# Performance work log

Hardware: AMD Instinct MI355X
Metric: run time of the kernel (lower is better)

## Reference

```python
import jax, jax.numpy as jnp
import numpy as np

B, S, H, NH, L, MLP_MULT = 4, 1024, 1024, 16, 2, 4
DK = H // NH
EPS = 1e-5


def setup_inputs() -> dict:
    key = jax.random.key(0)
    ks = jax.random.split(key, 8)
    p = lambda k, shape: jax.random.normal(k, shape, dtype=jnp.float32) * 0.02
    return {
        'hidden_states': jax.random.normal(ks[0], (B, S, H), dtype=jnp.float32),
        'attn_w': p(ks[1], (L, H, 3 * H)),
        'attn_b': jnp.zeros((L, 3 * H), jnp.float32),
        'proj_w': p(ks[2], (L, H, H)),
        'proj_b': jnp.zeros((L, H), jnp.float32),
        'fc_w': p(ks[3], (L, H, MLP_MULT * H)),
        'fc_b': jnp.zeros((L, MLP_MULT * H), jnp.float32),
        'fc2_w': p(ks[4], (L, MLP_MULT * H, H)),
        'fc2_b': jnp.zeros((L, H), jnp.float32),
        'ln1_g': jnp.ones((L, H), jnp.float32),
        'ln1_b': jnp.zeros((L, H), jnp.float32),
        'ln2_g': jnp.ones((L, H), jnp.float32),
        'ln2_b': jnp.zeros((L, H), jnp.float32),
        'position_ids': jnp.arange(S, dtype=jnp.int32),
    }


def _ln(x, g, b):
    m = jnp.mean(x, axis=-1, keepdims=True)
    v = jnp.var(x, axis=-1, keepdims=True)
    return (x - m) * jax.lax.rsqrt(v + EPS) * g + b


def _rotate_half(x):
    x1, x2 = jnp.split(x, 2, axis=-1)
    return jnp.concatenate((-x2, x1), axis=-1)


def _forward(hidden_states, attn_w, attn_b, proj_w, proj_b, fc_w, fc_b,
             fc2_w, fc2_b, ln1_g, ln1_b, ln2_g, ln2_b, position_ids):
    # rotary tables (fp32 math, as in RotaryEmbedding.forward)
    inv_freq = 1.0 / (10000.0 ** (jnp.arange(0, DK, 2, dtype=jnp.float32) / DK))
    freqs = position_ids.astype(jnp.float32)[:, None] * inv_freq[None, :]  # [S, DK/2]
    emb = jnp.concatenate((freqs, freqs), axis=-1)                          # [S, DK]
    cos = jnp.cos(emb)[None, None]  # [1,1,S,DK]
    sin = jnp.sin(emb)[None, None]
    causal = jnp.tril(jnp.ones((S, S), dtype=bool))
    neg = jnp.finfo(jnp.float32).min
    scale = 1.0 / np.sqrt(DK).astype(np.float32)

    h = hidden_states
    for i in range(L):
        # attention block
        x = _ln(h, ln1_g[i], ln1_b[i])
        qkv = x @ attn_w[i] + attn_b[i]                  # Conv1D c_attn
        q, k, v = jnp.split(qkv, 3, axis=-1)
        heads = lambda t: t.reshape(B, S, NH, DK).transpose(0, 2, 1, 3)
        q, k, v = heads(q), heads(k), heads(v)           # [B,NH,S,DK]
        q = q * cos + _rotate_half(q) * sin
        k = k * cos + _rotate_half(k) * sin
        # fp32 QK^T (baddbmm with alpha=scale, beta=0)
        w = jnp.einsum('bhqd,bhkd->bhqk', q.astype(jnp.float32),
                       k.astype(jnp.float32)) * scale    # [B,NH,S,S]
        w = jnp.where(causal, w, neg)
        w = jax.nn.softmax(w, axis=-1).astype(v.dtype)   # attn dropout is identity (eval)
        a = jnp.einsum('bhqk,bhkd->bhqd', w, v)
        a = a.transpose(0, 2, 1, 3).reshape(B, S, H)     # merge_heads
        h = h + (a @ proj_w[i] + proj_b[i])              # c_proj + residual
        # MLP block (gelu_new == tanh-approx gelu)
        x = _ln(h, ln2_g[i], ln2_b[i])
        mid = jax.nn.gelu(x @ fc_w[i] + fc_b[i], approximate=True)
        h = h + (mid @ fc2_w[i] + fc2_b[i])
    return h


def reference(hidden_states, attn_w, attn_b, proj_w, proj_b, fc_w, fc_b,
              fc2_w, fc2_b, ln1_g, ln1_b, ln2_g, ln2_b, position_ids):
    return _forward(hidden_states, attn_w, attn_b, proj_w, proj_b, fc_w, fc_b,
                    fc2_w, fc2_b, ln1_g, ln1_b, ln2_g, ln2_b, position_ids)
```

## Files before the change

### kernel.cpp

```cpp
#include <hip/hip_runtime.h>

#define B_ 4
#define S_ 1024
#define H_ 1024
#define NH_ 16
#define DK_ 64
#define MLPH_ 4096
#define EPS_ 1e-5f

typedef __attribute__((ext_vector_type(8))) short short8_t;
typedef __attribute__((ext_vector_type(8))) unsigned short ushort8_t;
typedef __attribute__((ext_vector_type(4))) float f32x4;

__device__ __forceinline__ unsigned short f2bf(float f) {
  unsigned int u = __float_as_uint(f);
  u = u + 0x7fffu + ((u >> 16) & 1u);
  return (unsigned short)(u >> 16);
}
__device__ __forceinline__ float bf2f(unsigned short b) {
  return __uint_as_float(((unsigned int)b) << 16);
}

__device__ __forceinline__ void gload16(const void* g, void* l) {
  typedef const __attribute__((address_space(1))) unsigned int GU;
  typedef __attribute__((address_space(3))) unsigned int LU;
  __builtin_amdgcn_global_load_lds((GU*)(size_t)g, (LU*)(unsigned int)(size_t)l, 16, 0, 0);
}

__device__ __forceinline__ float gelu_tanh(float x) {
  float y = 1.5957691216057308f * (x + 0.044715f * x * x * x);
  return x / (1.0f + __expf(-y));
}

__global__ __launch_bounds__(256) void wconv(const float* __restrict__ src,
                                             unsigned short* __restrict__ dst,
                                             int K, int N) {
  __shared__ float t[32][33];
  int n0 = blockIdx.x * 32, k0 = blockIdx.y * 32;
  int tid = threadIdx.x;
  int r = tid >> 3, c = (tid & 7) * 4;
  const float* s = src + (size_t)(k0 + r) * N + n0 + c;
  float4 v = *(const float4*)s;
  t[r][c] = v.x; t[r][c + 1] = v.y; t[r][c + 2] = v.z; t[r][c + 3] = v.w;
  __syncthreads();
  ushort4 o;
  o.x = f2bf(t[c + 0][r]); o.y = f2bf(t[c + 1][r]);
  o.z = f2bf(t[c + 2][r]); o.w = f2bf(t[c + 3][r]);
  *(ushort4*)(dst + (size_t)(n0 + r) * K + k0 + c) = o;
}

__global__ __launch_bounds__(256) void ln_kernel(const float* __restrict__ x,
                                                 const float* __restrict__ g,
                                                 const float* __restrict__ b,
                                                 unsigned short* __restrict__ y) {
  int row = blockIdx.x, tid = threadIdx.x;
  const float* xp = x + (size_t)row * H_;
  float4 v = *((const float4*)xp + tid);
  float s  = v.x + v.y + v.z + v.w;
  float s2 = v.x * v.x + v.y * v.y + v.z * v.z + v.w * v.w;
  #pragma unroll
  for (int o = 1; o < 64; o <<= 1) {
    s  += __shfl_xor(s, o, 64);
    s2 += __shfl_xor(s2, o, 64);
  }
  __shared__ float r1[4], r2[4];
  if ((tid & 63) == 0) { r1[tid >> 6] = s; r2[tid >> 6] = s2; }
  __syncthreads();
  s  = r1[0] + r1[1] + r1[2] + r1[3];
  s2 = r2[0] + r2[1] + r2[2] + r2[3];
  float mean = s * (1.0f / H_);
  float var  = s2 * (1.0f / H_) - mean * mean;
  float inv  = rsqrtf(var + EPS_);
  float4 gv = *((const float4*)g + tid);
  float4 bv = *((const float4*)b + tid);
  ushort4 o;
  o.x = f2bf((v.x - mean) * inv * gv.x + bv.x);
  o.y = f2bf((v.y - mean) * inv * gv.y + bv.y);
  o.z = f2bf((v.z - mean) * inv * gv.z + bv.z);
  o.w = f2bf((v.w - mean) * inv * gv.w + bv.w);
  *(ushort4*)(y + (size_t)row * H_ + tid * 4) = o;
}

__global__ __launch_bounds__(256) void rope_bf(unsigned short* qkv, const int* __restrict__ pos) {
  int idx = blockIdx.x * 256 + threadIdx.x;
  int d = idx & 31;
  int hh = (idx >> 5) & 15;
  int s = (idx >> 9) & 1023;
  int b = idx >> 19;
  size_t base = ((size_t)(b * S_ + s)) * 3072 + hh * 64;
  float inv = __expf(-9.210340371976184f * ((float)d * 0.03125f));
  float th = (float)pos[s] * inv;
  float cs = cosf(th), sn = sinf(th);
  unsigned short* qp = qkv + base;
  unsigned short* kp = qkv + base + 1024;
  float q0 = bf2f(qp[d]), q1 = bf2f(qp[d + 32]);
  float k0 = bf2f(kp[d]), k1 = bf2f(kp[d + 32]);
  qp[d]      = f2bf(q0 * cs - q1 * sn);
  qp[d + 32] = f2bf(q1 * cs + q0 * sn);
  kp[d]      = f2bf(k0 * cs - k1 * sn);
  kp[d + 32] = f2bf(k1 * cs + k0 * sn);
}

template <int MODE, int NT>
__global__ __launch_bounds__(256) void gemm_mfma(
    const unsigned short* __restrict__ A, const unsigned short* __restrict__ Bt,
    const float* __restrict__ bias, const float* __restrict__ resid,
    void* __restrict__ outp, int M, int N, int K) {
  constexpr int BN = NT * 32;
  constexpr int CB = BN / 32;
  __shared__ __align__(16) unsigned short As[2][128 * 64];
  __shared__ __align__(16) unsigned short Bs[2][BN * 64];
  int tid = threadIdx.x;
  int w = tid >> 6, lane = tid & 63;
  int m0 = blockIdx.y * 128, n0 = blockIdx.x * BN;
  int wr = w >> 1, wc = w & 1;
  int fr = lane & 15, kg = lane >> 4;
  f32x4 acc[4][NT];
  #pragma unroll
  for (int m = 0; m < 4; m++)
    #pragma unroll
    for (int n = 0; n < NT; n++) {
      acc[m][n][0] = 0.f; acc[m][n][1] = 0.f; acc[m][n][2] = 0.f; acc[m][n][3] = 0.f;
    }
  int srow = lane >> 3;
  int scol = ((lane & 7) ^ srow) * 8;
  const unsigned short* Ap = A  + (size_t)(m0 + w * 32 + srow) * K + scol;
  const unsigned short* Bp = Bt + (size_t)(n0 + w * (8 * CB) + srow) * K + scol;
  int sx = (fr & 7);
  int nk = K >> 6;
  {
    char* AsB = (char*)As[0] + w * 4096;
    char* BsB = (char*)Bs[0] + w * CB * 1024;
    #pragma unroll
    for (int i = 0; i < 4; i++) gload16(Ap + (size_t)i * 8 * K, AsB + i * 1024);
    #pragma unroll
    for (int i = 0; i < CB; i++) gload16(Bp + (size_t)i * 8 * K, BsB + i * 1024);
  }
  __syncthreads();
  for (int t = 0; t < nk; t++) {
    int cur = t & 1;
    if (t + 1 < nk) {
      const unsigned short* Ap2 = Ap + (size_t)(t + 1) * 64;
      const unsigned short* Bp2 = Bp + (size_t)(t + 1) * 64;
      char* AsB = (char*)As[cur ^ 1] + w * 4096;
      char* BsB = (char*)Bs[cur ^ 1] + w * CB * 1024;
      #pragma unroll
      for (int i = 0; i < 4; i++) gload16(Ap2 + (size_t)i * 8 * K, AsB + i * 1024);
      #pragma unroll
      for (int i = 0; i < CB; i++) gload16(Bp2 + (size_t)i * 8 * K, BsB + i * 1024);
    }
    #pragma unroll
    for (int kk = 0; kk < 2; kk++) {
      int slot = ((kk * 4 + kg) ^ sx) << 4;
      short8_t af[4], bfr[NT];
      #pragma unroll
      for (int m = 0; m < 4; m++)
        af[m] = *(const short8_t*)((char*)As[cur] + (wr * 64 + m * 16 + fr) * 128 + slot);
      #pragma unroll
      for (int n = 0; n < NT; n++)
        bfr[n] = *(const short8_t*)((char*)Bs[cur] + (wc * (NT * 16) + n * 16 + fr) * 128 + slot);
      #pragma unroll
      for (int m = 0; m < 4; m++)
        #pragma unroll
        for (int n = 0; n < NT; n++)
          acc[m][n] = __builtin_amdgcn_mfma_f32_16x16x32_bf16(af[m], bfr[n], acc[m][n], 0, 0, 0);
    }
    __syncthreads();
  }
  #pragma unroll
  for (int n = 0; n < NT; n++) {
    int col = n0 + wc * (NT * 16) + n * 16 + fr;
    float bv = bias[col];
    #pragma unroll
    for (int m = 0; m < 4; m++) {
      int row = m0 + wr * 64 + m * 16 + kg * 4;
      #pragma unroll
      for (int r = 0; r < 4; r++) {
        float v = acc[m][n][r] + bv;
        size_t idx = (size_t)(row + r) * N + col;
        if (MODE == 2)      ((float*)outp)[idx] = resid[idx] + v;
        else if (MODE == 1) ((unsigned short*)outp)[idx] = f2bf(gelu_tanh(v));
        else                ((unsigned short*)outp)[idx] = f2bf(v);
      }
    }
  }
}

__global__ __launch_bounds__(256) void attn3(const unsigned short* __restrict__ qkv,
                                             unsigned short* __restrict__ aout) {
  __shared__ __align__(16) unsigned short Ks[2][64 * 64];
  __shared__ __align__(16) unsigned short Vt[2][64 * 64];
  __shared__ __align__(16) unsigned short Ps[4][16 * 64];
  int tid = threadIdx.x;
  int w = tid >> 6, lane = tid & 63;
  int fr = lane & 15, kg = lane >> 4;
  int qt = (int)gridDim.x - 1 - (int)blockIdx.x;
  int q0 = qt * 64;
  int head = blockIdx.y, b = blockIdx.z;
  const unsigned short* base = qkv + ((size_t)b * S_) * 3072 + head * 64;

  const unsigned short* qp = base + (size_t)(q0 + w * 16 + fr) * 3072 + kg * 8;
  short8_t qa0 = *(const short8_t*)qp;
  short8_t qa1 = *(const short8_t*)(qp + 32);

  f32x4 acc[4];
  float mrun[4], lrun[4];
  #pragma unroll
  for (int n = 0; n < 4; n++) { acc[n][0] = 0.f; acc[n][1] = 0.f; acc[n][2] = 0.f; acc[n][3] = 0.f; }
  #pragma unroll
  for (int r = 0; r < 4; r++) { mrun[r] = -3.0e38f; lrun[r] = 0.f; }

  int skv = lane;
  int sd0 = w * 16;

  const unsigned short* kp0 = base + 1024 + (size_t)skv * 3072 + sd0;
  short8_t ka = *(const short8_t*)kp0;
  short8_t kb = *(const short8_t*)(kp0 + 8);
  short8_t va = *(const short8_t*)(kp0 + 1024);
  short8_t vb = *(const short8_t*)(kp0 + 1032);

  for (int t = 0; t <= qt; t++) {
    int cur = t & 1;
    {
      unsigned kbyte = skv * 128 + sd0 * 2;
      unsigned ksw = (skv & 7) << 4;
      *(short8_t*)((char*)Ks[cur] + (kbyte ^ ksw)) = ka;
      *(short8_t*)((char*)Ks[cur] + ((kbyte + 16) ^ ksw)) = kb;
      #pragma unroll
      for (int j = 0; j < 8; j++) {
        int d0 = sd0 + j, d1 = sd0 + 8 + j;
        *(unsigned short*)((char*)Vt[cur] + ((d0 * 128 + skv * 2) ^ ((d0 & 7) << 4))) = (unsigned short)va[j];
        *(unsigned short*)((char*)Vt[cur] + ((d1 * 128 + skv * 2) ^ ((d1 & 7) << 4))) = (unsigned short)vb[j];
      }
    }
    if (t < qt) {
      const unsigned short* kp = base + 1024 + (size_t)((t + 1) * 64 + skv) * 3072 + sd0;
      ka = *(const short8_t*)kp;
      kb = *(const short8_t*)(kp + 8);
      va = *(const short8_t*)(kp + 1024);
      vb = *(const short8_t*)(kp + 1032);
    }
    __syncthreads();
    f32x4 s[4];
    #pragma unroll
    for (int n = 0; n < 4; n++) {
      int kvrow = n * 16 + fr;
      unsigned sw = (kvrow & 7) << 4;
      short8_t b0 = *(const short8_t*)((char*)Ks[cur] + ((kvrow * 128 + kg * 16) ^ sw));
      short8_t b1 = *(const short8_t*)((char*)Ks[cur] + ((kvrow * 128 + 64 + kg * 16) ^ sw));
      f32x4 z; z[0] = 0.f; z[1] = 0.f; z[2] = 0.f; z[3] = 0.f;
      z = __builtin_amdgcn_mfma_f32_16x16x32_bf16(qa0, b0, z, 0, 0, 0);
      z = __builtin_amdgcn_mfma_f32_16x16x32_bf16(qa1, b1, z, 0, 0, 0);
      s[n] = z;
    }
    bool diag = (t == qt);
    float p[4][4], pmax[4];
    #pragma unroll
    for (int r = 0; r < 4; r++) {
      int qrow = w * 16 + kg * 4 + r;
      float rm = -3.0e38f;
      #pragma unroll
      for (int n = 0; n < 4; n++) {
        float sv = s[n][r] * 0.125f;
        if (diag && (n * 16 + fr > qrow)) sv = -3.0e38f;
        s[n][r] = sv;
        rm = fmaxf(rm, sv);
      }
      pmax[r] = rm;
    }
    bool need = (pmax[0] > mrun[0] + 8.f) | (pmax[1] > mrun[1] + 8.f) |
                (pmax[2] > mrun[2] + 8.f) | (pmax[3] > mrun[3] + 8.f);
    if (__any(need)) {
      #pragma unroll
      for (int r = 0; r < 4; r++) {
        float rm = pmax[r];
        rm = fmaxf(rm, __shfl_xor(rm, 1, 64));
        rm = fmaxf(rm, __shfl_xor(rm, 2, 64));
        rm = fmaxf(rm, __shfl_xor(rm, 4, 64));
        rm = fmaxf(rm, __shfl_xor(rm, 8, 64));
        float mn = fmaxf(mrun[r], rm);
        float sc = __expf(mrun[r] - mn);
        mrun[r] = mn;
        lrun[r] *= sc;
        #pragma unroll
        for (int n = 0; n < 4; n++) acc[n][r] *= sc;
      }
    }
    #pragma unroll
    for (int r = 0; r < 4; r++) {
      float ls = 0.f;
      #pragma unroll
      for (int n = 0; n < 4; n++) {
        float e = __expf(s[n][r] - mrun[r]);
        p[n][r] = e;
        ls += e;
      }
      lrun[r] += ls;
    }
    #pragma unroll
    for (int n = 0; n < 4; n++)
      #pragma unroll
      for (int r = 0; r < 4; r++) {
        int row = kg * 4 + r, col = n * 16 + fr;
        *(unsigned short*)((char*)Ps[w] + ((row * 128 + col * 2) ^ ((row & 7) << 4))) = f2bf(p[n][r]);
      }
    asm volatile("s_waitcnt lgkmcnt(0)" ::: "memory");
    unsigned psw = (fr & 7) << 4;
    short8_t pa0 = *(const short8_t*)((char*)Ps[w] + ((fr * 128 + kg * 16) ^ psw));
    short8_t pa1 = *(const short8_t*)((char*)Ps[w] + ((fr * 128 + 64 + kg * 16) ^ psw));
    #pragma unroll
    for (int n = 0; n < 4; n++) {
      int d = n * 16 + fr;
      unsigned sw = (d & 7) << 4;
      short8_t v0 = *(const short8_t*)((char*)Vt[cur] + ((d * 128 + kg * 16) ^ sw));
      short8_t v1 = *(const short8_t*)((char*)Vt[cur] + ((d * 128 + 64 + kg * 16) ^ sw));
      acc[n] = __builtin_amdgcn_mfma_f32_16x16x32_bf16(pa0, v0, acc[n], 0, 0, 0);
      acc[n] = __builtin_amdgcn_mfma_f32_16x16x32_bf16(pa1, v1, acc[n], 0, 0, 0);
    }
  }
  #pragma unroll
  for (int r = 0; r < 4; r++) {
    float ls = lrun[r];
    ls += __shfl_xor(ls, 1, 64);
    ls += __shfl_xor(ls, 2, 64);
    ls += __shfl_xor(ls, 4, 64);
    ls += __shfl_xor(ls, 8, 64);
    float inv = 1.0f / ls;
    size_t row = (size_t)b * S_ + q0 + w * 16 + kg * 4 + r;
    unsigned short* op = aout + row * H_ + head * 64 + fr;
    #pragma unroll
    for (int n = 0; n < 4; n++) op[n * 16] = f2bf(acc[n][r] * inv);
  }
}

extern "C" void kernel_launch(void* const* d_in, const int* in_sizes, int n_in,
                              void* d_out, int out_size, void* d_ws, size_t ws_size,
                              hipStream_t stream) {
  const float* hs     = (const float*)d_in[0];
  const float* attn_w = (const float*)d_in[1];
  const float* attn_b = (const float*)d_in[2];
  const float* proj_w = (const float*)d_in[3];
  const float* proj_b = (const float*)d_in[4];
  const float* fc_w   = (const float*)d_in[5];
  const float* fc_b   = (const float*)d_in[6];
  const float* fc2_w  = (const float*)d_in[7];
  const float* fc2_b  = (const float*)d_in[8];
  const float* ln1_g  = (const float*)d_in[9];
  const float* ln1_b  = (const float*)d_in[10];
  const float* ln2_g  = (const float*)d_in[11];
  const float* ln2_b  = (const float*)d_in[12];
  const int*   pos    = (const int*)d_in[13];

  float* hres = (float*)d_out;
  const size_t rows = (size_t)B_ * S_;

  unsigned short* wQ    = (unsigned short*)d_ws;
  unsigned short* wP    = wQ  + (size_t)2 * 3072 * 1024;
  unsigned short* wF1   = wP  + (size_t)2 * 1024 * 1024;
  unsigned short* wF2   = wF1 + (size_t)2 * 4096 * 1024;
  unsigned short* xbf   = wF2 + (size_t)2 * 1024 * 4096;
  unsigned short* qkvbf = xbf + rows * H_;
  unsigned short* midbf = qkvbf + rows * 3 * H_;
  unsigned short* aoutbf= midbf + rows * MLPH_;

  hipMemcpyAsync(hres, hs, rows * H_ * sizeof(float), hipMemcpyDeviceToDevice, stream);

  for (int l = 0; l < 2; l++) {
    wconv<<<dim3(96, 32), 256, 0, stream>>>(attn_w + (size_t)l * 1024 * 3072,
                                            wQ + (size_t)l * 3072 * 1024, 1024, 3072);
    wconv<<<dim3(32, 32), 256, 0, stream>>>(proj_w + (size_t)l * 1024 * 1024,
                                            wP + (size_t)l * 1024 * 1024, 1024, 1024);
    wconv<<<dim3(128, 32), 256, 0, stream>>>(fc_w + (size_t)l * 1024 * 4096,
                                             wF1 + (size_t)l * 4096 * 1024, 1024, 4096);
    wconv<<<dim3(32, 128), 256, 0, stream>>>(fc2_w + (size_t)l * 4096 * 1024,
                                             wF2 + (size_t)l * 1024 * 4096, 4096, 1024);
  }

  for (int l = 0; l < 2; l++) {
    ln_kernel<<<rows, 256, 0, stream>>>(hres, ln1_g + l * H_, ln1_b + l * H_, xbf);
    gemm_mfma<0, 4><<<dim3(24, 32), 256, 0, stream>>>(
        xbf, wQ + (size_t)l * 3072 * 1024, attn_b + (size_t)l * 3072, nullptr,
        qkvbf, 4096, 3072, 1024);
    rope_bf<<<8192, 256, 0, stream>>>(qkvbf, pos);
    attn3<<<dim3(16, 16, 4), 256, 0, stream>>>(qkvbf, aoutbf);
    gemm_mfma<2, 2><<<dim3(16, 32), 256, 0, stream>>>(
        aoutbf, wP + (size_t)l * 1024 * 1024, proj_b + (size_t)l * 1024, hres,
        hres, 4096, 1024, 1024);
    ln_kernel<<<rows, 256, 0, stream>>>(hres, ln2_g + l * H_, ln2_b + l * H_, xbf);
    gemm_mfma<1, 4><<<dim3(32, 32), 256, 0, stream>>>(
        xbf, wF1 + (size_t)l * 4096 * 1024, fc_b + (size_t)l * 4096, nullptr,
        midbf, 4096, 4096, 1024);
    gemm_mfma<2, 2><<<dim3(16, 32), 256, 0, stream>>>(
        midbf, wF2 + (size_t)l * 1024 * 4096, fc2_b + (size_t)l * 1024, hres,
        hres, 4096, 1024, 4096);
  }
}
```

Before: 478.7 us.

## Load K fragments directly to registers in attention, add XCD tile swizzle and setprio

The attention kernel drops the K shared-memory tile. Each wave now loads its own K MFMA fragments straight from global memory into registers and prefetches the next tile after the QK MFMAs, which removes LDS writes and reads for K. It also wraps the MFMA sections in s_setprio to favour the matrix work. Separately, the GEMM remaps block IDs with an 8-way XCD-aware swizzle to improve L2 locality of tiles across chiplets, at the cost of redundant K global loads across the four waves.

```diff
diff --git a/kernel.cpp b/kernel.cpp
--- a/kernel.cpp
+++ b/kernel.cpp
@@ -112,7 +112,12 @@
   __shared__ __align__(16) unsigned short Bs[2][BN * 64];
   int tid = threadIdx.x;
   int w = tid >> 6, lane = tid & 63;
-  int m0 = blockIdx.y * 128, n0 = blockIdx.x * BN;
+  int gx = gridDim.x;
+  int nwg = gx * gridDim.y;
+  int bid = blockIdx.y * gx + blockIdx.x;
+  int cpx = nwg >> 3;
+  int swz = (bid & 7) * cpx + (bid >> 3);
+  int m0 = (swz / gx) * 128, n0 = (swz % gx) * BN;
   int wr = w >> 1, wc = w & 1;
   int fr = lane & 15, kg = lane >> 4;
   f32x4 acc[4][NT];
@@ -186,9 +191,8 @@
   }
 }
 
-__global__ __launch_bounds__(256) void attn3(const unsigned short* __restrict__ qkv,
+__global__ __launch_bounds__(256) void attn4(const unsigned short* __restrict__ qkv,
                                              unsigned short* __restrict__ aout) {
-  __shared__ __align__(16) unsigned short Ks[2][64 * 64];
   __shared__ __align__(16) unsigned short Vt[2][64 * 64];
   __shared__ __align__(16) unsigned short Ps[4][16 * 64];
   int tid = threadIdx.x;
@@ -212,46 +216,53 @@
 
   int skv = lane;
   int sd0 = w * 16;
-
-  const unsigned short* kp0 = base + 1024 + (size_t)skv * 3072 + sd0;
-  short8_t ka = *(const short8_t*)kp0;
-  short8_t kb = *(const short8_t*)(kp0 + 8);
-  short8_t va = *(const short8_t*)(kp0 + 1024);
-  short8_t vb = *(const short8_t*)(kp0 + 1032);
+  const unsigned short* vbase = base + 2048;
+  const size_t KSTRIDE = (size_t)64 * 3072;
+
+  const unsigned short* kfp0 = base + 1024 + (size_t)(0 * 16 + fr) * 3072 + kg * 8;
+  const unsigned short* kfp1 = base + 1024 + (size_t)(1 * 16 + fr) * 3072 + kg * 8;
+  const unsigned short* kfp2 = base + 1024 + (size_t)(2 * 16 + fr) * 3072 + kg * 8;
+  const unsigned short* kfp3 = base + 1024 + (size_t)(3 * 16 + fr) * 3072 + kg * 8;
+
+  short8_t kf0[4], kf1[4];
+  kf0[0] = *(const short8_t*)kfp0;  kf1[0] = *(const short8_t*)(kfp0 + 32);
+  kf0[1] = *(const short8_t*)kfp1;  kf1[1] = *(const short8_t*)(kfp1 + 32);
+  kf0[2] = *(const short8_t*)kfp2;  kf1[2] = *(const short8_t*)(kfp2 + 32);
+  kf0[3] = *(const short8_t*)kfp3;  kf1[3] = *(const short8_t*)(kfp3 + 32);
+  const unsigned short* vp0 = vbase + (size_t)skv * 3072 + sd0;
+  short8_t va = *(const short8_t*)vp0;
+  short8_t vb = *(const short8_t*)(vp0 + 8);
 
   for (int t = 0; t <= qt; t++) {
     int cur = t & 1;
-    {
-      unsigned kbyte = skv * 128 + sd0 * 2;
-      unsigned ksw = (skv & 7) << 4;
-      *(short8_t*)((char*)Ks[cur] + (kbyte ^ ksw)) = ka;
-      *(short8_t*)((char*)Ks[cur] + ((kbyte + 16) ^ ksw)) = kb;
-      #pragma unroll
-      for (int j = 0; j < 8; j++) {
-        int d0 = sd0 + j, d1 = sd0 + 8 + j;
-        *(unsigned short*)((char*)Vt[cur] + ((d0 * 128 + skv * 2) ^ ((d0 & 7) << 4))) = (unsigned short)va[j];
-        *(unsigned short*)((char*)Vt[cur] + ((d1 * 128 + skv * 2) ^ ((d1 & 7) << 4))) = (unsigned short)vb[j];
-      }
+    #pragma unroll
+    for (int j = 0; j < 8; j++) {
+      int d0 = sd0 + j, d1 = sd0 + 8 + j;
+      *(unsigned short*)((char*)Vt[cur] + ((d0 * 128 + skv * 2) ^ ((d0 & 7) << 4))) = (unsigned short)va[j];
+      *(unsigned short*)((char*)Vt[cur] + ((d1 * 128 + skv * 2) ^ ((d1 & 7) << 4))) = (unsigned short)vb[j];
     }
     if (t < qt) {
-      const unsigned short* kp = base + 1024 + (size_t)((t + 1) * 64 + skv) * 3072 + sd0;
-      ka = *(const short8_t*)kp;
-      kb = *(const short8_t*)(kp + 8);
-      va = *(const short8_t*)(kp + 1024);
-      vb = *(const short8_t*)(kp + 1032);
+      const unsigned short* vp = vbase + (size_t)((t + 1) * 64 + skv) * 3072 + sd0;
+      va = *(const short8_t*)vp;
+      vb = *(const short8_t*)(vp + 8);
     }
     __syncthreads();
+    __builtin_amdgcn_s_setprio(1);
     f32x4 s[4];
     #pragma unroll
     for (int n = 0; n < 4; n++) {
-      int kvrow = n * 16 + fr;
-      unsigned sw = (kvrow & 7) << 4;
-      short8_t b0 = *(const short8_t*)((char*)Ks[cur] + ((kvrow * 128 + kg * 16) ^ sw));
-      short8_t b1 = *(const short8_t*)((char*)Ks[cur] + ((kvrow * 128 + 64 + kg * 16) ^ sw));
       f32x4 z; z[0] = 0.f; z[1] = 0.f; z[2] = 0.f; z[3] = 0.f;
-      z = __builtin_amdgcn_mfma_f32_16x16x32_bf16(qa0, b0, z, 0, 0, 0);
-      z = __builtin_amdgcn_mfma_f32_16x16x32_bf16(qa1, b1, z, 0, 0, 0);
+      z = __builtin_amdgcn_mfma_f32_16x16x32_bf16(qa0, kf0[n], z, 0, 0, 0);
+      z = __builtin_amdgcn_mfma_f32_16x16x32_bf16(qa1, kf1[n], z, 0, 0, 0);
       s[n] = z;
+    }
+    __builtin_amdgcn_s_setprio(0);
+    if (t < qt) {
+      size_t off = (size_t)(t + 1) * KSTRIDE;
+      kf0[0] = *(const short8_t*)(kfp0 + off);  kf1[0] = *(const short8_t*)(kfp0 + off + 32);
+      kf0[1] = *(const short8_t*)(kfp1 + off);  kf1[1] = *(const short8_t*)(kfp1 + off + 32);
+      kf0[2] = *(const short8_t*)(kfp2 + off);  kf1[2] = *(const short8_t*)(kfp2 + off + 32);
+      kf0[3] = *(const short8_t*)(kfp3 + off);  kf1[3] = *(const short8_t*)(kfp3 + off + 32);
     }
     bool diag = (t == qt);
     float p[4][4], pmax[4];
@@ -308,6 +319,7 @@
     unsigned psw = (fr & 7) << 4;
     short8_t pa0 = *(const short8_t*)((char*)Ps[w] + ((fr * 128 + kg * 16) ^ psw));
     short8_t pa1 = *(const short8_t*)((char*)Ps[w] + ((fr * 128 + 64 + kg * 16) ^ psw));
+    __builtin_amdgcn_s_setprio(1);
     #pragma unroll
     for (int n = 0; n < 4; n++) {
       int d = n * 16 + fr;
@@ -317,6 +329,7 @@
       acc[n] = __builtin_amdgcn_mfma_f32_16x16x32_bf16(pa0, v0, acc[n], 0, 0, 0);
       acc[n] = __builtin_amdgcn_mfma_f32_16x16x32_bf16(pa1, v1, acc[n], 0, 0, 0);
     }
+    __builtin_amdgcn_s_setprio(0);
   }
   #pragma unroll
   for (int r = 0; r < 4; r++) {
@@ -382,7 +395,7 @@
         xbf, wQ + (size_t)l * 3072 * 1024, attn_b + (size_t)l * 3072, nullptr,
         qkvbf, 4096, 3072, 1024);
     rope_bf<<<8192, 256, 0, stream>>>(qkvbf, pos);
-    attn3<<<dim3(16, 16, 4), 256, 0, stream>>>(qkvbf, aoutbf);
+    attn4<<<dim3(16, 16, 4), 256, 0, stream>>>(qkvbf, aoutbf);
     gemm_mfma<2, 2><<<dim3(16, 32), 256, 0, stream>>>(
         aoutbf, wP + (size_t)l * 1024 * 1024, proj_b + (size_t)l * 1024, hres,
         hres, 4096, 1024, 1024);
```

New measurement: 523.6 us. 1.09x slower.

## Enlarge attention query tile to 128 rows and swizzle GEMM workgroups across XCDs

Applied to the files above, without the earlier changes.

The attention kernel now gives each block 128 query rows, two 16-row groups per wave, so each K/V tile staged in shared memory is reused by twice as many MFMAs, and the grid is halved. MFMA sections are wrapped in s_setprio to favour matrix issue. The GEMM remaps block IDs in groups of eight so consecutive tiles land on the same XCD for better L2 locality. In exchange the attention kernel uses more registers and has fewer blocks, which can hurt occupancy and causal load balance.

```diff
diff --git a/kernel.cpp b/kernel.cpp
--- a/kernel.cpp
+++ b/kernel.cpp
@@ -112,7 +112,12 @@
   __shared__ __align__(16) unsigned short Bs[2][BN * 64];
   int tid = threadIdx.x;
   int w = tid >> 6, lane = tid & 63;
-  int m0 = blockIdx.y * 128, n0 = blockIdx.x * BN;
+  int gx = gridDim.x;
+  int nwg = gx * gridDim.y;
+  int bid = blockIdx.y * gx + blockIdx.x;
+  int cpx = nwg >> 3;
+  int swz = (bid & 7) * cpx + (bid >> 3);
+  int m0 = (swz / gx) * 128, n0 = (swz % gx) * BN;
   int wr = w >> 1, wc = w & 1;
   int fr = lane & 15, kg = lane >> 4;
   f32x4 acc[4][NT];
@@ -186,29 +191,36 @@
   }
 }
 
-__global__ __launch_bounds__(256) void attn3(const unsigned short* __restrict__ qkv,
+__global__ __launch_bounds__(256) void attn5(const unsigned short* __restrict__ qkv,
                                              unsigned short* __restrict__ aout) {
   __shared__ __align__(16) unsigned short Ks[2][64 * 64];
   __shared__ __align__(16) unsigned short Vt[2][64 * 64];
-  __shared__ __align__(16) unsigned short Ps[4][16 * 64];
+  __shared__ __align__(16) unsigned short Ps[4][2][16 * 64];
   int tid = threadIdx.x;
   int w = tid >> 6, lane = tid & 63;
   int fr = lane & 15, kg = lane >> 4;
   int qt = (int)gridDim.x - 1 - (int)blockIdx.x;
-  int q0 = qt * 64;
+  int q0 = qt * 128;
   int head = blockIdx.y, b = blockIdx.z;
   const unsigned short* base = qkv + ((size_t)b * S_) * 3072 + head * 64;
 
-  const unsigned short* qp = base + (size_t)(q0 + w * 16 + fr) * 3072 + kg * 8;
-  short8_t qa0 = *(const short8_t*)qp;
-  short8_t qa1 = *(const short8_t*)(qp + 32);
-
-  f32x4 acc[4];
-  float mrun[4], lrun[4];
-  #pragma unroll
-  for (int n = 0; n < 4; n++) { acc[n][0] = 0.f; acc[n][1] = 0.f; acc[n][2] = 0.f; acc[n][3] = 0.f; }
-  #pragma unroll
-  for (int r = 0; r < 4; r++) { mrun[r] = -3.0e38f; lrun[r] = 0.f; }
+  short8_t qa0[2], qa1[2];
+  #pragma unroll
+  for (int g = 0; g < 2; g++) {
+    const unsigned short* qp = base + (size_t)(q0 + w * 32 + g * 16 + fr) * 3072 + kg * 8;
+    qa0[g] = *(const short8_t*)qp;
+    qa1[g] = *(const short8_t*)(qp + 32);
+  }
+
+  f32x4 acc[2][4];
+  float mrun[2][4], lrun[2][4];
+  #pragma unroll
+  for (int g = 0; g < 2; g++)
+    #pragma unroll
+    for (int n = 0; n < 4; n++) {
+      acc[g][n][0] = 0.f; acc[g][n][1] = 0.f; acc[g][n][2] = 0.f; acc[g][n][3] = 0.f;
+      mrun[g][n] = -3.0e38f; lrun[g][n] = 0.f;
+    }
 
   int skv = lane;
   int sd0 = w * 16;
@@ -219,7 +231,8 @@
   short8_t va = *(const short8_t*)(kp0 + 1024);
   short8_t vb = *(const short8_t*)(kp0 + 1032);
 
-  for (int t = 0; t <= qt; t++) {
+  int ntiles = 2 * qt + 2;
+  for (int t = 0; t < ntiles; t++) {
     int cur = t & 1;
     {
       unsigned kbyte = skv * 128 + sd0 * 2;
@@ -233,7 +246,7 @@
         *(unsigned short*)((char*)Vt[cur] + ((d1 * 128 + skv * 2) ^ ((d1 & 7) << 4))) = (unsigned short)vb[j];
       }
     }
-    if (t < qt) {
+    if (t + 1 < ntiles) {
       const unsigned short* kp = base + 1024 + (size_t)((t + 1) * 64 + skv) * 3072 + sd0;
       ka = *(const short8_t*)kp;
       kb = *(const short8_t*)(kp + 8);
@@ -241,96 +254,121 @@
       vb = *(const short8_t*)(kp + 1032);
     }
     __syncthreads();
-    f32x4 s[4];
-    #pragma unroll
-    for (int n = 0; n < 4; n++) {
-      int kvrow = n * 16 + fr;
-      unsigned sw = (kvrow & 7) << 4;
-      short8_t b0 = *(const short8_t*)((char*)Ks[cur] + ((kvrow * 128 + kg * 16) ^ sw));
-      short8_t b1 = *(const short8_t*)((char*)Ks[cur] + ((kvrow * 128 + 64 + kg * 16) ^ sw));
-      f32x4 z; z[0] = 0.f; z[1] = 0.f; z[2] = 0.f; z[3] = 0.f;
-      z = __builtin_amdgcn_mfma_f32_16x16x32_bf16(qa0, b0, z, 0, 0, 0);
-      z = __builtin_amdgcn_mfma_f32_16x16x32_bf16(qa1, b1, z, 0, 0, 0);
-      s[n] = z;
-    }
-    bool diag = (t == qt);
-    float p[4][4], pmax[4];
-    #pragma unroll
-    for (int r = 0; r < 4; r++) {
-      int qrow = w * 16 + kg * 4 + r;
-      float rm = -3.0e38f;
+    f32x4 s[2][4];
+    {
+      short8_t b0[4], b1[4];
       #pragma unroll
       for (int n = 0; n < 4; n++) {
-        float sv = s[n][r] * 0.125f;
-        if (diag && (n * 16 + fr > qrow)) sv = -3.0e38f;
-        s[n][r] = sv;
-        rm = fmaxf(rm, sv);
-      }
-      pmax[r] = rm;
-    }
-    bool need = (pmax[0] > mrun[0] + 8.f) | (pmax[1] > mrun[1] + 8.f) |
-                (pmax[2] > mrun[2] + 8.f) | (pmax[3] > mrun[3] + 8.f);
+        int kvrow = n * 16 + fr;
+        unsigned sw = (kvrow & 7) << 4;
+        b0[n] = *(const short8_t*)((char*)Ks[cur] + ((kvrow * 128 + kg * 16) ^ sw));
+        b1[n] = *(const short8_t*)((char*)Ks[cur] + ((kvrow * 128 + 64 + kg * 16) ^ sw));
+      }
+      __builtin_amdgcn_s_setprio(1);
+      #pragma unroll
+      for (int g = 0; g < 2; g++)
+        #pragma unroll
+        for (int n = 0; n < 4; n++) {
+          f32x4 z; z[0] = 0.f; z[1] = 0.f; z[2] = 0.f; z[3] = 0.f;
+          z = __builtin_amdgcn_mfma_f32_16x16x32_bf16(qa0[g], b0[n], z, 0, 0, 0);
+          z = __builtin_amdgcn_mfma_f32_16x16x32_bf16(qa1[g], b1[n], z, 0, 0, 0);
+          s[g][n] = z;
+        }
+      __builtin_amdgcn_s_setprio(0);
+    }
+    bool diag = (t >= 2 * qt);
+    float pmax[2][4];
+    #pragma unroll
+    for (int g = 0; g < 2; g++)
+      #pragma unroll
+      for (int r = 0; r < 4; r++) {
+        int qrow = q0 + w * 32 + g * 16 + kg * 4 + r;
+        float rm = -3.0e38f;
+        #pragma unroll
+        for (int n = 0; n < 4; n++) {
+          float sv = s[g][n][r] * 0.125f;
+          if (diag && (t * 64 + n * 16 + fr > qrow)) sv = -3.0e38f;
+          s[g][n][r] = sv;
+          rm = fmaxf(rm, sv);
+        }
+        pmax[g][r] = rm;
+      }
+    bool need = false;
+    #pragma unroll
+    for (int g = 0; g < 2; g++)
+      #pragma unroll
+      for (int r = 0; r < 4; r++) need |= (pmax[g][r] > mrun[g][r] + 8.f);
     if (__any(need)) {
       #pragma unroll
+      for (int g = 0; g < 2; g++)
+        #pragma unroll
+        for (int r = 0; r < 4; r++) {
+          float rm = pmax[g][r];
+          rm = fmaxf(rm, __shfl_xor(rm, 1, 64));
+          rm = fmaxf(rm, __shfl_xor(rm, 2, 64));
+          rm = fmaxf(rm, __shfl_xor(rm, 4, 64));
+          rm = fmaxf(rm, __shfl_xor(rm, 8, 64));
+          float mn = fmaxf(mrun[g][r], rm);
+          float sc = __expf(mrun[g][r] - mn);
+          mrun[g][r] = mn;
+          lrun[g][r] *= sc;
+          #pragma unroll
+          for (int n = 0; n < 4; n++) acc[g][n][r] *= sc;
+        }
+    }
+    #pragma unroll
+    for (int g = 0; g < 2; g++)
+      #pragma unroll
       for (int r = 0; r < 4; r++) {
-        float rm = pmax[r];
-        rm = fmaxf(rm, __shfl_xor(rm, 1, 64));
-        rm = fmaxf(rm, __shfl_xor(rm, 2, 64));
-        rm = fmaxf(rm, __shfl_xor(rm, 4, 64));
-        rm = fmaxf(rm, __shfl_xor(rm, 8, 64));
-        float mn = fmaxf(mrun[r], rm);
-        float sc = __expf(mrun[r] - mn);
-        mrun[r] = mn;
-        lrun[r] *= sc;
+        float ls = 0.f;
+        int row = kg * 4 + r;
         #pragma unroll
-        for (int n = 0; n < 4; n++) acc[n][r] *= sc;
-      }
-    }
-    #pragma unroll
-    for (int r = 0; r < 4; r++) {
-      float ls = 0.f;
-      #pragma unroll
-      for (int n = 0; n < 4; n++) {
-        float e = __expf(s[n][r] - mrun[r]);
-        p[n][r] = e;
-        ls += e;
-      }
-      lrun[r] += ls;
-    }
-    #pragma unroll
-    for (int n = 0; n < 4; n++)
-      #pragma unroll
-      for (int r = 0; r < 4; r++) {
-        int row = kg * 4 + r, col = n * 16 + fr;
-        *(unsigned short*)((char*)Ps[w] + ((row * 128 + col * 2) ^ ((row & 7) << 4))) = f2bf(p[n][r]);
+        for (int n = 0; n < 4; n++) {
+          float e = __expf(s[g][n][r] - mrun[g][r]);
+          ls += e;
+          int col = n * 16 + fr;
+          *(unsigned short*)((char*)Ps[w][g] + ((row * 128 + col * 2) ^ ((row & 7) << 4))) = f2bf(e);
+        }
+        lrun[g][r] += ls;
       }
     asm volatile("s_waitcnt lgkmcnt(0)" ::: "memory");
     unsigned psw = (fr & 7) << 4;
-    short8_t pa0 = *(const short8_t*)((char*)Ps[w] + ((fr * 128 + kg * 16) ^ psw));
-    short8_t pa1 = *(const short8_t*)((char*)Ps[w] + ((fr * 128 + 64 + kg * 16) ^ psw));
+    short8_t pa0[2], pa1[2];
+    #pragma unroll
+    for (int g = 0; g < 2; g++) {
+      pa0[g] = *(const short8_t*)((char*)Ps[w][g] + ((fr * 128 + kg * 16) ^ psw));
+      pa1[g] = *(const short8_t*)((char*)Ps[w][g] + ((fr * 128 + 64 + kg * 16) ^ psw));
+    }
+    __builtin_amdgcn_s_setprio(1);
     #pragma unroll
     for (int n = 0; n < 4; n++) {
       int d = n * 16 + fr;
       unsigned sw = (d & 7) << 4;
       short8_t v0 = *(const short8_t*)((char*)Vt[cur] + ((d * 128 + kg * 16) ^ sw));
       short8_t v1 = *(const short8_t*)((char*)Vt[cur] + ((d * 128 + 64 + kg * 16) ^ sw));
-      acc[n] = __builtin_amdgcn_mfma_f32_16x16x32_bf16(pa0, v0, acc[n], 0, 0, 0);
-      acc[n] = __builtin_amdgcn_mfma_f32_16x16x32_bf16(pa1, v1, acc[n], 0, 0, 0);
-    }
-  }
-  #pragma unroll
-  for (int r = 0; r < 4; r++) {
-    float ls = lrun[r];
-    ls += __shfl_xor(ls, 1, 64);
-    ls += __shfl_xor(ls, 2, 64);
-    ls += __shfl_xor(ls, 4, 64);
-    ls += __shfl_xor(ls, 8, 64);
-    float inv = 1.0f / ls;
-    size_t row = (size_t)b * S_ + q0 + w * 16 + kg * 4 + r;
-    unsigned short* op = aout + row * H_ + head * 64 + fr;
-    #pragma unroll
-    for (int n = 0; n < 4; n++) op[n * 16] = f2bf(acc[n][r] * inv);
-  }
+      #pragma unroll
+      for (int g = 0; g < 2; g++) {
+        acc[g][n] = __builtin_amdgcn_mfma_f32_16x16x32_bf16(pa0[g], v0, acc[g][n], 0, 0, 0);
+        acc[g][n] = __builtin_amdgcn_mfma_f32_16x16x32_bf16(pa1[g], v1, acc[g][n], 0, 0, 0);
+      }
+    }
+    __builtin_amdgcn_s_setprio(0);
+  }
+  #pragma unroll
+  for (int g = 0; g < 2; g++)
+    #pragma unroll
+    for (int r = 0; r < 4; r++) {
+      float ls = lrun[g][r];
+      ls += __shfl_xor(ls, 1, 64);
+      ls += __shfl_xor(ls, 2, 64);
+      ls += __shfl_xor(ls, 4, 64);
+      ls += __shfl_xor(ls, 8, 64);
+      float inv = 1.0f / ls;
+      size_t row = (size_t)b * S_ + q0 + w * 32 + g * 16 + kg * 4 + r;
+      unsigned short* op = aout + row * H_ + head * 64 + fr;
+      #pragma unroll
+      for (int n = 0; n < 4; n++) op[n * 16] = f2bf(acc[g][n][r] * inv);
+    }
 }
 
 extern "C" void kernel_launch(void* const* d_in, const int* in_sizes, int n_in,
@@ -382,7 +420,7 @@
         xbf, wQ + (size_t)l * 3072 * 1024, attn_b + (size_t)l * 3072, nullptr,
         qkvbf, 4096, 3072, 1024);
     rope_bf<<<8192, 256, 0, stream>>>(qkvbf, pos);
-    attn3<<<dim3(16, 16, 4), 256, 0, stream>>>(qkvbf, aoutbf);
+    attn5<<<dim3(8, 16, 4), 256, 0, stream>>>(qkvbf, aoutbf);
     gemm_mfma<2, 2><<<dim3(16, 32), 256, 0, stream>>>(
         aoutbf, wP + (size_t)l * 1024 * 1024, proj_b + (size_t)l * 1024, hres,
         hres, 4096, 1024, 1024);
```

New measurement: 466.2 us. 1.03x faster.
